# Kernel tuning notes

Measured on AMD Instinct MI355X. Metric: run time of the kernel, lower is better.

The kernel has to match this reference:

```python
import jax, jax.numpy as jnp
import numpy as np

S = 30.0   # arcface scale
M = 0.4    # arcface angular margin
EPS = 1e-7

def setup_inputs() -> dict:
    key = jax.random.key(0)
    k1, k2, k3 = jax.random.split(key, 3)
    N, D, C = 4096, 512, 50000
    x = jax.random.normal(k1, (N, D), dtype=jnp.float32)
    # fc weight [out_fts, in_fts]; note the original's normalize loop is a no-op,
    # so W is used UN-normalized in the matmul.
    W = jax.random.normal(k2, (C, D), dtype=jnp.float32) * 0.02
    target = jax.random.randint(k3, (N,), 0, C, dtype=jnp.int32)
    return {"x": x, "W": W, "target": target}

def reference(x, W, target):
    # L2-normalize embeddings along feature dim (p=2, dim=1)
    xn = x / jnp.linalg.norm(x, axis=1, keepdims=True)
    # logits [N, C] = normalized_input @ W^T (W not normalized; see note)
    logits = jnp.einsum('nd,cd->nc', xn, W)
    # target cosine per row: diagonal(logits.T[target]) == logits[i, target[i]]
    tgt = jnp.take_along_axis(logits, target[:, None].astype(jnp.int32), axis=1)[:, 0]
    # arcface numerator: s * cos(acos(clamp(cos_t)) + m)
    numerator = S * jnp.cos(jnp.arccos(jnp.clip(tgt, -1.0 + EPS, 1.0 - EPS)) + M)
    # excl: all classes except the target column; masked exp-sum
    C = logits.shape[1]
    mask = jnp.arange(C, dtype=jnp.int32)[None, :] != target[:, None]  # [N, C]
    excl_sum = jnp.sum(jnp.where(mask, jnp.exp(S * logits), 0.0), axis=1)
    denominator = jnp.exp(numerator) + excl_sum
    L = numerator - jnp.log(denominator)
    return -jnp.mean(L)
```

## Files before the change

### kernel.cpp

```cpp
#include <hip/hip_runtime.h>
#include <hip/hip_bf16.h>

typedef __attribute__((ext_vector_type(8))) short bf16x8;
typedef __attribute__((ext_vector_type(4))) float f32x4;
typedef __attribute__((address_space(1))) const void glob_cv;
typedef __attribute__((address_space(3))) void lds_v;

constexpr int N_ = 4096, D_ = 512, C_ = 50000;
constexpr float S_ = 30.0f, M_ = 0.4f, EPS_ = 1e-7f;

__device__ inline ushort f2bf(float f) {
  unsigned u = __builtin_bit_cast(unsigned, f);
  u += 0x7fffu + ((u >> 16) & 1u);
  return (ushort)(u >> 16);
}

__global__ __launch_bounds__(256) void convw_kernel(const float* __restrict__ W,
                                                    ushort* __restrict__ Wb) {
  const long total = (long)C_ * D_ / 8;
  const long stride = (long)gridDim.x * 256;
  for (long k = (long)blockIdx.x * 256 + threadIdx.x; k < total; k += stride) {
    float4 a = reinterpret_cast<const float4*>(W)[2 * k];
    float4 b = reinterpret_cast<const float4*>(W)[2 * k + 1];
    union { ushort u[8]; uint4 v; } pk;
    pk.u[0] = f2bf(a.x); pk.u[1] = f2bf(a.y); pk.u[2] = f2bf(a.z); pk.u[3] = f2bf(a.w);
    pk.u[4] = f2bf(b.x); pk.u[5] = f2bf(b.y); pk.u[6] = f2bf(b.z); pk.u[7] = f2bf(b.w);
    reinterpret_cast<uint4*>(Wb)[k] = pk.v;
  }
}

__global__ __launch_bounds__(256) void norm_kernel(const float* __restrict__ x,
                                                   ushort* __restrict__ xnb) {
  const int wid = threadIdx.x >> 6;
  const int lane = threadIdx.x & 63;
  const int row = blockIdx.x * 4 + wid;
  const float4* xr = reinterpret_cast<const float4*>(x + (size_t)row * D_);
  float4 a = xr[lane * 2];
  float4 b = xr[lane * 2 + 1];
  float ss = a.x * a.x + a.y * a.y + a.z * a.z + a.w * a.w +
             b.x * b.x + b.y * b.y + b.z * b.z + b.w * b.w;
#pragma unroll
  for (int m = 1; m < 64; m <<= 1) ss += __shfl_xor(ss, m);
  const float inv = 1.0f / sqrtf(ss);
  union { ushort u[8]; uint4 v; } pk;
  pk.u[0] = f2bf(a.x * inv); pk.u[1] = f2bf(a.y * inv);
  pk.u[2] = f2bf(a.z * inv); pk.u[3] = f2bf(a.w * inv);
  pk.u[4] = f2bf(b.x * inv); pk.u[5] = f2bf(b.y * inv);
  pk.u[6] = f2bf(b.z * inv); pk.u[7] = f2bf(b.w * inv);
  reinterpret_cast<uint4*>(xnb + (size_t)row * D_)[lane] = pk.v;
}

__global__ __launch_bounds__(256) void gemm_fast(
    const ushort* __restrict__ A,
    const ushort* __restrict__ Wb,
    const int* __restrict__ target,
    float* __restrict__ row_sum,
    float* __restrict__ tgt_logit) {
  __shared__ char As[16384];
  __shared__ char Bs[16384];
  __shared__ int tgt_s[128];

  const int t = threadIdx.x, lane = t & 63, wid = t >> 6;
  const int wr = wid >> 1, wc = wid & 1;
  const int row0 = blockIdx.x * 128, col0 = blockIdx.y * 128;
  if (t < 128) tgt_s[t] = target[row0 + t];

  const int rsub = lane >> 3;
  const int kel = ((lane & 7) ^ rsub) << 3;

  f32x4 acc[4][4] = {};

  for (int kt = 0; kt < D_ / 64; ++kt) {
    __syncthreads();
#pragma unroll
    for (int i = 0; i < 4; ++i) {
      const int q = wid * 4 + i;
      const int r = q * 8 + rsub;
      const ushort* srcA = A + (size_t)(row0 + r) * D_ + kt * 64 + kel;
      __builtin_amdgcn_global_load_lds((glob_cv*)srcA, (lds_v*)(As + q * 1024), 16, 0, 0);
      const int gc = col0 + r;
      const ushort* srcB = Wb + (size_t)(gc < C_ ? gc : 0) * D_ + kt * 64 + kel;
      __builtin_amdgcn_global_load_lds((glob_cv*)srcB, (lds_v*)(Bs + q * 1024), 16, 0, 0);
    }
    __syncthreads();
#pragma unroll
    for (int h = 0; h < 2; ++h) {
      const int kbh = h * 64 + ((lane >> 4) << 4);
      const int swz = (lane & 7) << 4;
      bf16x8 af[4], bfr[4];
#pragma unroll
      for (int m = 0; m < 4; ++m) {
        const int r = wr * 64 + m * 16 + (lane & 15);
        af[m] = *reinterpret_cast<const bf16x8*>(As + r * 128 + (kbh ^ swz));
      }
#pragma unroll
      for (int n = 0; n < 4; ++n) {
        const int c = wc * 64 + n * 16 + (lane & 15);
        bfr[n] = *reinterpret_cast<const bf16x8*>(Bs + c * 128 + (kbh ^ swz));
      }
#pragma unroll
      for (int m = 0; m < 4; ++m)
#pragma unroll
        for (int n = 0; n < 4; ++n)
          acc[m][n] = __builtin_amdgcn_mfma_f32_16x16x32_bf16(af[m], bfr[n], acc[m][n], 0, 0, 0);
    }
  }

#pragma unroll
  for (int m = 0; m < 4; ++m) {
#pragma unroll
    for (int j = 0; j < 4; ++j) {
      const int lr = wr * 64 + m * 16 + ((lane >> 4) << 2) + j;
      const int grow = row0 + lr;
      const int trow = tgt_s[lr];
      float s = 0.f;
#pragma unroll
      for (int n = 0; n < 4; ++n) {
        const int gcol = col0 + wc * 64 + n * 16 + (lane & 15);
        const float v = acc[m][n][j];
        if (gcol < C_) s += __expf(S_ * v);
        if (gcol == trow) tgt_logit[grow] = v;
      }
      s += __shfl_xor(s, 1); s += __shfl_xor(s, 2);
      s += __shfl_xor(s, 4); s += __shfl_xor(s, 8);
      if ((lane & 15) == 0) atomicAdd(&row_sum[grow], s);
    }
  }
}

__global__ __launch_bounds__(256) void gemm_kernel(
    const ushort* __restrict__ A, const float* __restrict__ W,
    const int* __restrict__ target, float* __restrict__ row_sum,
    float* __restrict__ tgt_logit) {
  constexpr int BM = 128, BN = 128, BK = 64;
  __shared__ char As[BM * BK * 2];
  __shared__ char Bs[BN * BK * 2];
  __shared__ int tgt_s[BM];
  const int t = threadIdx.x;
  const int lane = t & 63, wid = t >> 6;
  const int wr = wid >> 1, wc = wid & 1;
  const int row0 = blockIdx.x * BM;
  const int col0 = blockIdx.y * BN;
  if (t < BM) tgt_s[t] = target[row0 + t];
  f32x4 acc[4][4] = {};
  for (int kt = 0; kt < D_ / BK; ++kt) {
    __syncthreads();
#pragma unroll
    for (int i = 0; i < 4; ++i) {
      const int L = i * 4096 + t * 16;
      const int r = L >> 7, kb = L & 127;
      const char* gsrc = reinterpret_cast<const char*>(A) +
                         (size_t)(row0 + r) * (D_ * 2) + kt * (BK * 2) + kb;
      uint4 v = *reinterpret_cast<const uint4*>(gsrc);
      *reinterpret_cast<uint4*>(As + r * 128 + (kb ^ ((r & 7) << 4))) = v;
    }
#pragma unroll
    for (int j = 0; j < 8; ++j) {
      const int flat = j * 256 + t;
      const int c = flat >> 4, kq = flat & 15;
      const int gc = col0 + c;
      float4 v = make_float4(0.f, 0.f, 0.f, 0.f);
      if (gc < C_)
        v = *reinterpret_cast<const float4*>(W + (size_t)gc * D_ + kt * BK + kq * 4);
      ushort4 h;
      h.x = f2bf(v.x); h.y = f2bf(v.y); h.z = f2bf(v.z); h.w = f2bf(v.w);
      const int kb = kq * 8;
      *reinterpret_cast<ushort4*>(Bs + c * 128 + (kb ^ ((c & 7) << 4))) = h;
    }
    __syncthreads();
#pragma unroll
    for (int h = 0; h < 2; ++h) {
      const int kbh = h * 64 + ((lane >> 4) << 4);
      bf16x8 af[4], bfr[4];
#pragma unroll
      for (int m = 0; m < 4; ++m) {
        const int r = wr * 64 + m * 16 + (lane & 15);
        af[m] = *reinterpret_cast<const bf16x8*>(As + r * 128 + (kbh ^ ((r & 7) << 4)));
      }
#pragma unroll
      for (int n = 0; n < 4; ++n) {
        const int c = wc * 64 + n * 16 + (lane & 15);
        bfr[n] = *reinterpret_cast<const bf16x8*>(Bs + c * 128 + (kbh ^ ((c & 7) << 4)));
      }
#pragma unroll
      for (int m = 0; m < 4; ++m)
#pragma unroll
        for (int n = 0; n < 4; ++n)
          acc[m][n] = __builtin_amdgcn_mfma_f32_16x16x32_bf16(af[m], bfr[n], acc[m][n], 0, 0, 0);
    }
  }
#pragma unroll
  for (int m = 0; m < 4; ++m) {
#pragma unroll
    for (int j = 0; j < 4; ++j) {
      const int lr = wr * 64 + m * 16 + ((lane >> 4) << 2) + j;
      const int grow = row0 + lr;
      const int trow = tgt_s[lr];
      float s = 0.f;
#pragma unroll
      for (int n = 0; n < 4; ++n) {
        const int gcol = col0 + wc * 64 + n * 16 + (lane & 15);
        const float v = acc[m][n][j];
        if (gcol < C_) s += __expf(S_ * v);
        if (gcol == trow) tgt_logit[grow] = v;
      }
      s += __shfl_xor(s, 1); s += __shfl_xor(s, 2);
      s += __shfl_xor(s, 4); s += __shfl_xor(s, 8);
      if ((lane & 15) == 0) atomicAdd(&row_sum[grow], s);
    }
  }
}

__global__ __launch_bounds__(256) void loss_kernel(const float* __restrict__ row_sum,
                                                   const float* __restrict__ tgt_logit,
                                                   float* __restrict__ out) {
  __shared__ float red[4];
  float acc = 0.f;
  for (int i = threadIdx.x; i < N_; i += 256) {
    const float tv = tgt_logit[i];
    const float tc = fminf(fmaxf(tv, -1.0f + EPS_), 1.0f - EPS_);
    const float num = S_ * cosf(acosf(tc) + M_);
    const float excl = row_sum[i] - __expf(S_ * tv);
    const float den = __expf(num) + excl;
    acc += num - logf(den);
  }
#pragma unroll
  for (int m = 1; m < 64; m <<= 1) acc += __shfl_xor(acc, m);
  if ((threadIdx.x & 63) == 0) red[threadIdx.x >> 6] = acc;
  __syncthreads();
  if (threadIdx.x == 0) out[0] = -(red[0] + red[1] + red[2] + red[3]) / (float)N_;
}

extern "C" void kernel_launch(void* const* d_in, const int* in_sizes, int n_in,
                              void* d_out, int out_size, void* d_ws, size_t ws_size,
                              hipStream_t stream) {
  const float* x = (const float*)d_in[0];
  const float* W = (const float*)d_in[1];
  const int* target = (const int*)d_in[2];
  float* out = (float*)d_out;

  float* row_sum = (float*)d_ws;
  float* tgt_logit = row_sum + N_;
  ushort* xnb = (ushort*)(row_sum + 2 * N_);
  ushort* Wb = xnb + (size_t)N_ * D_;

  const size_t need = 2 * N_ * sizeof(float) + (size_t)N_ * D_ * 2 + (size_t)C_ * D_ * 2;

  hipMemsetAsync(d_ws, 0, 2 * N_ * sizeof(float), stream);
  norm_kernel<<<N_ / 4, 256, 0, stream>>>(x, xnb);
  if (ws_size >= need) {
    convw_kernel<<<2048, 256, 0, stream>>>(W, Wb);
    gemm_fast<<<dim3(N_ / 128, (C_ + 127) / 128), 256, 0, stream>>>(
        xnb, Wb, target, row_sum, tgt_logit);
  } else {
    gemm_kernel<<<dim3(N_ / 128, (C_ + 127) / 128), 256, 0, stream>>>(
        xnb, W, target, row_sum, tgt_logit);
  }
  loss_kernel<<<1, 256, 0, stream>>>(row_sum, tgt_logit, out);
}
```

Baseline: 524.1 us.

## Pipeline GEMM with triple-buffered LDS, 256x128 tiles, and grid swizzle

Replaces the single-buffered 128x128 GEMM with a 512-thread 256x128-tile kernel. It prefetches two K-stages ahead into three LDS buffers and uses explicit vmcnt waits, raw barriers and setprio around the MFMA block to overlap global loads with compute. A block-index swizzle groups blocks that share W columns so they can reuse them through L2. The loss kernel is spread over 16 blocks that combine results with an atomic add into a zeroed output. The costs are much higher LDS use (144KB per block), which limits occupancy, and a loss sum whose result depends on atomic ordering.

```diff
diff --git a/kernel.cpp b/kernel.cpp
--- a/kernel.cpp
+++ b/kernel.cpp
@@ -8,6 +8,8 @@
 
 constexpr int N_ = 4096, D_ = 512, C_ = 50000;
 constexpr float S_ = 30.0f, M_ = 0.4f, EPS_ = 1e-7f;
+
+#define WAITVM(N) asm volatile("s_waitcnt vmcnt(" #N ")" ::: "memory")
 
 __device__ inline ushort f2bf(float f) {
   unsigned u = __builtin_bit_cast(unsigned, f);
@@ -50,61 +52,98 @@
   reinterpret_cast<uint4*>(xnb + (size_t)row * D_)[lane] = pk.v;
 }
 
-__global__ __launch_bounds__(256) void gemm_fast(
+__global__ __launch_bounds__(512, 2) void gemm_deep(
     const ushort* __restrict__ A,
     const ushort* __restrict__ Wb,
     const int* __restrict__ target,
     float* __restrict__ row_sum,
     float* __restrict__ tgt_logit) {
-  __shared__ char As[16384];
-  __shared__ char Bs[16384];
-  __shared__ int tgt_s[128];
+  __shared__ char As[3][256 * 128];
+  __shared__ char Bs[3][128 * 128];
+  __shared__ int tgt_s[256];
 
   const int t = threadIdx.x, lane = t & 63, wid = t >> 6;
   const int wr = wid >> 1, wc = wid & 1;
-  const int row0 = blockIdx.x * 128, col0 = blockIdx.y * 128;
-  if (t < 128) tgt_s[t] = target[row0 + t];
+
+  const int orig = blockIdx.y * 16 + blockIdx.x;
+  const int swz = (orig & 7) * 782 + (orig >> 3);
+  const int bx = swz & 15, by = swz >> 4;
+  const int row0 = bx * 256, col0 = by * 128;
+
+  if (t < 256) tgt_s[t] = target[row0 + t];
 
   const int rsub = lane >> 3;
   const int kel = ((lane & 7) ^ rsub) << 3;
 
-  f32x4 acc[4][4] = {};
-
-  for (int kt = 0; kt < D_ / 64; ++kt) {
-    __syncthreads();
+  auto STAGE = [&](int kt, int buf) {
 #pragma unroll
     for (int i = 0; i < 4; ++i) {
       const int q = wid * 4 + i;
       const int r = q * 8 + rsub;
-      const ushort* srcA = A + (size_t)(row0 + r) * D_ + kt * 64 + kel;
-      __builtin_amdgcn_global_load_lds((glob_cv*)srcA, (lds_v*)(As + q * 1024), 16, 0, 0);
+      const ushort* src = A + (size_t)(row0 + r) * D_ + kt * 64 + kel;
+      __builtin_amdgcn_global_load_lds((glob_cv*)src, (lds_v*)(&As[buf][q * 1024]), 16, 0, 0);
+    }
+#pragma unroll
+    for (int i = 0; i < 2; ++i) {
+      const int q = wid * 2 + i;
+      const int r = q * 8 + rsub;
       const int gc = col0 + r;
-      const ushort* srcB = Wb + (size_t)(gc < C_ ? gc : 0) * D_ + kt * 64 + kel;
-      __builtin_amdgcn_global_load_lds((glob_cv*)srcB, (lds_v*)(Bs + q * 1024), 16, 0, 0);
-    }
-    __syncthreads();
-#pragma unroll
-    for (int h = 0; h < 2; ++h) {
-      const int kbh = h * 64 + ((lane >> 4) << 4);
-      const int swz = (lane & 7) << 4;
-      bf16x8 af[4], bfr[4];
-#pragma unroll
-      for (int m = 0; m < 4; ++m) {
-        const int r = wr * 64 + m * 16 + (lane & 15);
-        af[m] = *reinterpret_cast<const bf16x8*>(As + r * 128 + (kbh ^ swz));
-      }
-#pragma unroll
-      for (int n = 0; n < 4; ++n) {
-        const int c = wc * 64 + n * 16 + (lane & 15);
-        bfr[n] = *reinterpret_cast<const bf16x8*>(Bs + c * 128 + (kbh ^ swz));
-      }
+      const ushort* src = Wb + (size_t)(gc < C_ ? gc : 0) * D_ + kt * 64 + kel;
+      __builtin_amdgcn_global_load_lds((glob_cv*)src, (lds_v*)(&Bs[buf][q * 1024]), 16, 0, 0);
+    }
+  };
+
+  f32x4 acc[4][4] = {};
+
+  STAGE(0, 0);
+  STAGE(1, 1);
+
+#pragma unroll
+  for (int kt = 0; kt < 8; ++kt) {
+    if (kt + 2 < 8) STAGE(kt + 2, (kt + 2) % 3);
+    if (kt < 6)       { WAITVM(12); }
+    else if (kt == 6) { WAITVM(6); }
+    else              { WAITVM(0); }
+    __builtin_amdgcn_s_barrier();
+    __builtin_amdgcn_sched_barrier(0);
+
+    const int buf = kt % 3;
+    const char* Ab = As[buf];
+    const char* Bb = Bs[buf];
+    const int kb0 = (lane >> 4) << 4;
+    bf16x8 af[4][2], bfr[4][2];
+#pragma unroll
+    for (int m = 0; m < 4; ++m) {
+      const int r = wr * 64 + m * 16 + (lane & 15);
+      const int sw = (r & 7) << 4;
+#pragma unroll
+      for (int h = 0; h < 2; ++h)
+        af[m][h] = *reinterpret_cast<const bf16x8*>(Ab + r * 128 + ((h * 64 + kb0) ^ sw));
+    }
+#pragma unroll
+    for (int n = 0; n < 4; ++n) {
+      const int c = wc * 64 + n * 16 + (lane & 15);
+      const int sw = (c & 7) << 4;
+#pragma unroll
+      for (int h = 0; h < 2; ++h)
+        bfr[n][h] = *reinterpret_cast<const bf16x8*>(Bb + c * 128 + ((h * 64 + kb0) ^ sw));
+    }
+
+    __builtin_amdgcn_s_setprio(1);
+#pragma unroll
+    for (int h = 0; h < 2; ++h)
 #pragma unroll
       for (int m = 0; m < 4; ++m)
 #pragma unroll
         for (int n = 0; n < 4; ++n)
-          acc[m][n] = __builtin_amdgcn_mfma_f32_16x16x32_bf16(af[m], bfr[n], acc[m][n], 0, 0, 0);
-    }
-  }
+          acc[m][n] = __builtin_amdgcn_mfma_f32_16x16x32_bf16(af[m][h], bfr[n][h], acc[m][n], 0, 0, 0);
+    __builtin_amdgcn_s_setprio(0);
+
+    __builtin_amdgcn_sched_barrier(0);
+    __builtin_amdgcn_s_barrier();
+  }
+
+  __syncthreads();
 
 #pragma unroll
   for (int m = 0; m < 4; ++m) {
@@ -215,20 +254,19 @@
                                                    const float* __restrict__ tgt_logit,
                                                    float* __restrict__ out) {
   __shared__ float red[4];
-  float acc = 0.f;
-  for (int i = threadIdx.x; i < N_; i += 256) {
-    const float tv = tgt_logit[i];
-    const float tc = fminf(fmaxf(tv, -1.0f + EPS_), 1.0f - EPS_);
-    const float num = S_ * cosf(acosf(tc) + M_);
-    const float excl = row_sum[i] - __expf(S_ * tv);
-    const float den = __expf(num) + excl;
-    acc += num - logf(den);
-  }
+  const int i = blockIdx.x * 256 + threadIdx.x;
+  const float tv = tgt_logit[i];
+  const float tc = fminf(fmaxf(tv, -1.0f + EPS_), 1.0f - EPS_);
+  const float num = S_ * cosf(acosf(tc) + M_);
+  const float excl = row_sum[i] - __expf(S_ * tv);
+  const float den = __expf(num) + excl;
+  float acc = num - logf(den);
 #pragma unroll
   for (int m = 1; m < 64; m <<= 1) acc += __shfl_xor(acc, m);
   if ((threadIdx.x & 63) == 0) red[threadIdx.x >> 6] = acc;
   __syncthreads();
-  if (threadIdx.x == 0) out[0] = -(red[0] + red[1] + red[2] + red[3]) / (float)N_;
+  if (threadIdx.x == 0)
+    atomicAdd(out, -(red[0] + red[1] + red[2] + red[3]) / (float)N_);
 }
 
 extern "C" void kernel_launch(void* const* d_in, const int* in_sizes, int n_in,
@@ -247,14 +285,15 @@
   const size_t need = 2 * N_ * sizeof(float) + (size_t)N_ * D_ * 2 + (size_t)C_ * D_ * 2;
 
   hipMemsetAsync(d_ws, 0, 2 * N_ * sizeof(float), stream);
+  hipMemsetAsync(d_out, 0, sizeof(float), stream);
   norm_kernel<<<N_ / 4, 256, 0, stream>>>(x, xnb);
   if (ws_size >= need) {
     convw_kernel<<<2048, 256, 0, stream>>>(W, Wb);
-    gemm_fast<<<dim3(N_ / 128, (C_ + 127) / 128), 256, 0, stream>>>(
+    gemm_deep<<<dim3(16, (C_ + 127) / 128), 512, 0, stream>>>(
         xnb, Wb, target, row_sum, tgt_logit);
   } else {
     gemm_kernel<<<dim3(N_ / 128, (C_ + 127) / 128), 256, 0, stream>>>(
         xnb, W, target, row_sum, tgt_logit);
   }
-  loss_kernel<<<1, 256, 0, stream>>>(row_sum, tgt_logit, out);
-}
+  loss_kernel<<<N_ / 256, 256, 0, stream>>>(row_sum, tgt_logit, out);
+}
```

Result: faster. 488.4 us (-6.8%).

## Replace GEMM with 256x256 double-buffered 8-phase pipelined kernel and parallel loss

Applied to the files above, without the earlier changes.

Swaps the 128x128 single-buffered bf16 MFMA GEMM for a 512-thread, 256x256-tile kernel. It double-buffers LDS (128KB), interleaves async global-to-LDS loads with MFMA phases using explicit vmcnt waits, barriers and setprio, and remaps block indices in a swizzled order for better L2 reuse. The goal is to hide load latency behind compute and raise arithmetic intensity, at the cost of more LDS per block and tighter occupancy. The loss kernel now runs over 16 blocks and combines results with an atomic add into a zeroed output, which makes the floating-point summation order non-deterministic.

```diff
diff --git a/kernel.cpp b/kernel.cpp
--- a/kernel.cpp
+++ b/kernel.cpp
@@ -8,6 +8,9 @@
 
 constexpr int N_ = 4096, D_ = 512, C_ = 50000;
 constexpr float S_ = 30.0f, M_ = 0.4f, EPS_ = 1e-7f;
+
+#define WAITVM(N) asm volatile("s_waitcnt vmcnt(" #N ")" ::: "memory")
+#define SBAR() do { __builtin_amdgcn_sched_barrier(0); __builtin_amdgcn_s_barrier(); __builtin_amdgcn_sched_barrier(0); } while (0)
 
 __device__ inline ushort f2bf(float f) {
   unsigned u = __builtin_bit_cast(unsigned, f);
@@ -50,74 +53,107 @@
   reinterpret_cast<uint4*>(xnb + (size_t)row * D_)[lane] = pk.v;
 }
 
-__global__ __launch_bounds__(256) void gemm_fast(
+__global__ __launch_bounds__(512, 2) void gemm_8ph(
     const ushort* __restrict__ A,
     const ushort* __restrict__ Wb,
     const int* __restrict__ target,
     float* __restrict__ row_sum,
     float* __restrict__ tgt_logit) {
-  __shared__ char As[16384];
-  __shared__ char Bs[16384];
-  __shared__ int tgt_s[128];
+  __shared__ char S[131072];
+  __shared__ int tgt_s[256];
 
   const int t = threadIdx.x, lane = t & 63, wid = t >> 6;
-  const int wr = wid >> 1, wc = wid & 1;
-  const int row0 = blockIdx.x * 128, col0 = blockIdx.y * 128;
-  if (t < 128) tgt_s[t] = target[row0 + t];
-
-  const int rsub = lane >> 3;
-  const int kel = ((lane & 7) ^ rsub) << 3;
-
-  f32x4 acc[4][4] = {};
-
-  for (int kt = 0; kt < D_ / 64; ++kt) {
-    __syncthreads();
-#pragma unroll
-    for (int i = 0; i < 4; ++i) {
-      const int q = wid * 4 + i;
-      const int r = q * 8 + rsub;
-      const ushort* srcA = A + (size_t)(row0 + r) * D_ + kt * 64 + kel;
-      __builtin_amdgcn_global_load_lds((glob_cv*)srcA, (lds_v*)(As + q * 1024), 16, 0, 0);
-      const int gc = col0 + r;
-      const ushort* srcB = Wb + (size_t)(gc < C_ ? gc : 0) * D_ + kt * 64 + kel;
-      __builtin_amdgcn_global_load_lds((glob_cv*)srcB, (lds_v*)(Bs + q * 1024), 16, 0, 0);
-    }
-    __syncthreads();
-#pragma unroll
-    for (int h = 0; h < 2; ++h) {
-      const int kbh = h * 64 + ((lane >> 4) << 4);
-      const int swz = (lane & 7) << 4;
-      bf16x8 af[4], bfr[4];
-#pragma unroll
-      for (int m = 0; m < 4; ++m) {
-        const int r = wr * 64 + m * 16 + (lane & 15);
-        af[m] = *reinterpret_cast<const bf16x8*>(As + r * 128 + (kbh ^ swz));
-      }
-#pragma unroll
-      for (int n = 0; n < 4; ++n) {
-        const int c = wc * 64 + n * 16 + (lane & 15);
-        bfr[n] = *reinterpret_cast<const bf16x8*>(Bs + c * 128 + (kbh ^ swz));
-      }
-#pragma unroll
-      for (int m = 0; m < 4; ++m)
-#pragma unroll
-        for (int n = 0; n < 4; ++n)
-          acc[m][n] = __builtin_amdgcn_mfma_f32_16x16x32_bf16(af[m], bfr[n], acc[m][n], 0, 0, 0);
-    }
-  }
-
-#pragma unroll
-  for (int m = 0; m < 4; ++m) {
+  const int wr = wid >> 2, wc = wid & 3;
+
+  const int orig = blockIdx.y * 16 + blockIdx.x;
+  const int swz = (orig & 7) * 392 + (orig >> 3);
+  const int row0 = (swz & 15) * 256, col0 = (swz >> 4) * 256;
+
+  const int ke = ((lane & 3) ^ ((lane >> 3) & 3)) << 3;
+  const int kb0 = (lane >> 4) << 4;
+
+  auto STG = [&](int T, int kh, int isB, int buf) {
+    char* dst = S + buf * 65536 + isB * 32768 + kh * 16384 + wid * 1024;
+#pragma unroll
+    for (int j = 0; j < 2; ++j) {
+      const int r = j * 128 + wid * 16 + (lane >> 2);
+      const ushort* src;
+      if (isB) {
+        const int gc = col0 + r;
+        src = Wb + (size_t)(gc < C_ ? gc : 0) * D_ + T * 64 + kh * 32 + ke;
+      } else {
+        src = A + (size_t)(row0 + r) * D_ + T * 64 + kh * 32 + ke;
+      }
+      __builtin_amdgcn_global_load_lds((glob_cv*)src, (lds_v*)(dst + j * 8192), 16, 0, 0);
+    }
+  };
+
+  f32x4 acc[8][4] = {};
+  bf16x8 bf[4];
+
+  auto PHASE = [&](int buf, int kh, int mh, auto stageFn, int wk) {
+    if (mh == 0) {
+      const char* Bb = S + buf * 65536 + 32768 + kh * 16384;
+#pragma unroll
+      for (int n = 0; n < 4; ++n) {
+        const int rc = wc * 64 + n * 16 + (lane & 15);
+        bf[n] = *reinterpret_cast<const bf16x8*>(Bb + rc * 64 + (kb0 ^ (((rc >> 1) & 3) << 4)));
+      }
+    }
+    const char* Ab = S + buf * 65536 + kh * 16384;
+    bf16x8 af[4];
+#pragma unroll
+    for (int mi = 0; mi < 4; ++mi) {
+      const int rr = wr * 128 + mh * 64 + mi * 16 + (lane & 15);
+      af[mi] = *reinterpret_cast<const bf16x8*>(Ab + rr * 64 + (kb0 ^ (((rr >> 1) & 3) << 4)));
+    }
+    stageFn();
+    SBAR();
+    __builtin_amdgcn_s_setprio(1);
+#pragma unroll
+    for (int mi = 0; mi < 4; ++mi)
+#pragma unroll
+      for (int n = 0; n < 4; ++n)
+        acc[mh * 4 + mi][n] =
+            __builtin_amdgcn_mfma_f32_16x16x32_bf16(af[mi], bf[n], acc[mh * 4 + mi][n], 0, 0, 0);
+    __builtin_amdgcn_s_setprio(0);
+    if (wk == 1) { WAITVM(4); }
+    else if (wk == 2) { WAITVM(0); }
+    SBAR();
+  };
+
+  STG(0, 0, 0, 0); STG(0, 0, 1, 0); STG(0, 1, 0, 0); STG(0, 1, 1, 0);
+  STG(1, 0, 0, 1); STG(1, 0, 1, 1);
+  WAITVM(4);
+  SBAR();
+
+#pragma unroll
+  for (int i = 0; i < 4; ++i) {
+    PHASE(0, 0, 0, [&] { STG(2 * i + 1, 1, 0, 1); }, 0);
+    PHASE(0, 0, 1, [&] { STG(2 * i + 1, 1, 1, 1); }, 0);
+    PHASE(0, 1, 0, [&] { if (i < 3) STG(2 * i + 2, 0, 0, 0); }, 0);
+    PHASE(0, 1, 1, [&] { if (i < 3) STG(2 * i + 2, 0, 1, 0); }, i < 3 ? 1 : 2);
+    PHASE(1, 0, 0, [&] { if (i < 3) STG(2 * i + 2, 1, 0, 0); }, 0);
+    PHASE(1, 0, 1, [&] { if (i < 3) STG(2 * i + 2, 1, 1, 0); }, 0);
+    PHASE(1, 1, 0, [&] { if (i < 3) STG(2 * i + 3, 0, 0, 1); }, 0);
+    PHASE(1, 1, 1, [&] { if (i < 3) STG(2 * i + 3, 0, 1, 1); }, i < 3 ? 1 : 2);
+  }
+
+  if (t < 256) tgt_s[t] = target[row0 + t];
+  __syncthreads();
+
+#pragma unroll
+  for (int mm = 0; mm < 8; ++mm) {
 #pragma unroll
     for (int j = 0; j < 4; ++j) {
-      const int lr = wr * 64 + m * 16 + ((lane >> 4) << 2) + j;
+      const int lr = wr * 128 + mm * 16 + ((lane >> 4) << 2) + j;
       const int grow = row0 + lr;
       const int trow = tgt_s[lr];
       float s = 0.f;
 #pragma unroll
       for (int n = 0; n < 4; ++n) {
         const int gcol = col0 + wc * 64 + n * 16 + (lane & 15);
-        const float v = acc[m][n][j];
+        const float v = acc[mm][n][j];
         if (gcol < C_) s += __expf(S_ * v);
         if (gcol == trow) tgt_logit[grow] = v;
       }
@@ -215,20 +251,19 @@
                                                    const float* __restrict__ tgt_logit,
                                                    float* __restrict__ out) {
   __shared__ float red[4];
-  float acc = 0.f;
-  for (int i = threadIdx.x; i < N_; i += 256) {
-    const float tv = tgt_logit[i];
-    const float tc = fminf(fmaxf(tv, -1.0f + EPS_), 1.0f - EPS_);
-    const float num = S_ * cosf(acosf(tc) + M_);
-    const float excl = row_sum[i] - __expf(S_ * tv);
-    const float den = __expf(num) + excl;
-    acc += num - logf(den);
-  }
+  const int i = blockIdx.x * 256 + threadIdx.x;
+  const float tv = tgt_logit[i];
+  const float tc = fminf(fmaxf(tv, -1.0f + EPS_), 1.0f - EPS_);
+  const float num = S_ * cosf(acosf(tc) + M_);
+  const float excl = row_sum[i] - __expf(S_ * tv);
+  const float den = __expf(num) + excl;
+  float acc = num - logf(den);
 #pragma unroll
   for (int m = 1; m < 64; m <<= 1) acc += __shfl_xor(acc, m);
   if ((threadIdx.x & 63) == 0) red[threadIdx.x >> 6] = acc;
   __syncthreads();
-  if (threadIdx.x == 0) out[0] = -(red[0] + red[1] + red[2] + red[3]) / (float)N_;
+  if (threadIdx.x == 0)
+    atomicAdd(out, -(red[0] + red[1] + red[2] + red[3]) / (float)N_);
 }
 
 extern "C" void kernel_launch(void* const* d_in, const int* in_sizes, int n_in,
@@ -247,14 +282,14 @@
   const size_t need = 2 * N_ * sizeof(float) + (size_t)N_ * D_ * 2 + (size_t)C_ * D_ * 2;
 
   hipMemsetAsync(d_ws, 0, 2 * N_ * sizeof(float), stream);
+  hipMemsetAsync(d_out, 0, sizeof(float), stream);
   norm_kernel<<<N_ / 4, 256, 0, stream>>>(x, xnb);
   if (ws_size >= need) {
     convw_kernel<<<2048, 256, 0, stream>>>(W, Wb);
-    gemm_fast<<<dim3(N_ / 128, (C_ + 127) / 128), 256, 0, stream>>>(
-        xnb, Wb, target, row_sum, tgt_logit);
+    gemm_8ph<<<dim3(16, 196), 512, 0, stream>>>(xnb, Wb, target, row_sum, tgt_logit);
   } else {
     gemm_kernel<<<dim3(N_ / 128, (C_ + 127) / 128), 256, 0, stream>>>(
         xnb, W, target, row_sum, tgt_logit);
   }
-  loss_kernel<<<1, 256, 0, stream>>>(row_sum, tgt_logit, out);
-}
+  loss_kernel<<<N_ / 256, 256, 0, stream>>>(row_sum, tgt_logit, out);
+}
```

Result: faster. 495.7 us (-5.4%).
